# Kernel optimization log

Measured on AMD Instinct MI355X. Metric: run time of the kernel, lower is better.

Reference implementation:

```python
import jax, jax.numpy as jnp
import numpy as np
import math

D_MODEL = 768
N_HEAD = 12
D_FF = 3072
LN_EPS = 1e-5


def gelu_new(x):
    return 0.5 * x * (1.0 + jnp.tanh(jnp.sqrt(2.0 / jnp.pi) * (x + 0.044715 * x ** 3)))


def layer_norm(x, g, b):
    mu = jnp.mean(x, axis=-1, keepdims=True)
    var = jnp.mean(jnp.square(x - mu), axis=-1, keepdims=True)
    return (x - mu) * jax.lax.rsqrt(var + LN_EPS) * g + b


def setup_inputs() -> dict:
    key = jax.random.key(0)
    ks = jax.random.split(key, 8)
    B, S = 4, 2048
    x = jax.random.normal(ks[0], (B, S, D_MODEL), dtype=jnp.float32)
    # causal look-ahead mask: 1 = attend, 0 = masked
    look_ahead_mask = jnp.tril(jnp.ones((S, S), dtype=jnp.float32))[None, None]
    std = 0.02
    Wqkv = jax.random.normal(ks[1], (D_MODEL, 3 * D_MODEL), dtype=jnp.float32) * std
    bqkv = jnp.zeros((3 * D_MODEL,), dtype=jnp.float32)
    Wo = jax.random.normal(ks[2], (D_MODEL, D_MODEL), dtype=jnp.float32) * std
    bo = jnp.zeros((D_MODEL,), dtype=jnp.float32)
    Wfc = jax.random.normal(ks[3], (D_MODEL, D_FF), dtype=jnp.float32) * std
    bfc = jnp.zeros((D_FF,), dtype=jnp.float32)
    Wpr = jax.random.normal(ks[4], (D_FF, D_MODEL), dtype=jnp.float32) * std
    bpr = jnp.zeros((D_MODEL,), dtype=jnp.float32)
    g1 = jnp.ones((D_MODEL,), dtype=jnp.float32)
    b1 = jnp.zeros((D_MODEL,), dtype=jnp.float32)
    g2 = jnp.ones((D_MODEL,), dtype=jnp.float32)
    b2 = jnp.zeros((D_MODEL,), dtype=jnp.float32)
    return dict(x=x, look_ahead_mask=look_ahead_mask, Wqkv=Wqkv, bqkv=bqkv,
                Wo=Wo, bo=bo, Wfc=Wfc, bfc=bfc, Wpr=Wpr, bpr=bpr,
                g1=g1, b1=b1, g2=g2, b2=b2)


def reference(x, look_ahead_mask, Wqkv, bqkv, Wo, bo, Wfc, bfc, Wpr, bpr, g1, b1, g2, b2):
    B, S, D = x.shape
    dk = D // N_HEAD
    # --- attention sublayer (dropout = identity, eval mode) ---
    nx = layer_norm(x, g1, b1)
    qkv = nx @ Wqkv + bqkv                       # [B,S,3D]
    q, k, v = jnp.split(qkv, 3, axis=-1)
    def heads(t):
        return t.reshape(B, S, N_HEAD, dk).transpose(0, 2, 1, 3)  # [B,H,S,dk]
    q, k, v = heads(q), heads(k), heads(v)
    scores = jnp.einsum('bhqd,bhkd->bhqk', q, k) / jnp.sqrt(jnp.float32(dk))
    scores = scores + (1.0 - look_ahead_mask) * -10000.0
    attn_scores = jax.nn.softmax(scores, axis=-1)  # [B,H,S,S]
    out = jnp.einsum('bhqk,bhkd->bhqd', attn_scores, v)
    out = out.transpose(0, 2, 1, 3).reshape(B, S, D)
    a = out @ Wo + bo
    x = x + a
    # --- MLP sublayer ---
    h = layer_norm(x, g2, b2)
    m = gelu_new(h @ Wfc + bfc) @ Wpr + bpr
    x = x + m
    return (x, attn_scores)
```

## Files before the change

kernel.cpp:

```cpp
#include <hip/hip_runtime.h>
#include <stdint.h>

#define D_MODEL 768
#define NHEAD   12
#define DKH     64
#define SEQ     2048
#define BATCH   4
#define DFF     3072
#define NROWS   (BATCH*SEQ)

typedef __bf16 bf16x8 __attribute__((ext_vector_type(8)));
typedef float  f32x4  __attribute__((ext_vector_type(4)));

__device__ __forceinline__ unsigned short f2bf(float f) {
  union { float f; unsigned int u; } v; v.f = f;
  unsigned int r = v.u + 0x7fffu + ((v.u >> 16) & 1u);
  return (unsigned short)(r >> 16);
}

__device__ __forceinline__ void gl_lds16(const void* g, void* l) {
  __builtin_amdgcn_global_load_lds(
      (__attribute__((address_space(1))) void*)(uintptr_t)g,
      (__attribute__((address_space(3))) void*)(uintptr_t)l, 16, 0, 0);
}

__global__ __launch_bounds__(256) void k_prep(
    const float* __restrict__ Wqkv, const float* __restrict__ Wo,
    const float* __restrict__ Wfc, const float* __restrict__ Wpr,
    unsigned short* __restrict__ WqkvT, unsigned short* __restrict__ WoT,
    unsigned short* __restrict__ WfcT, unsigned short* __restrict__ WprT,
    const float* __restrict__ x, const float* __restrict__ g1,
    const float* __restrict__ b1, unsigned short* __restrict__ nx) {
  int id = blockIdx.x;
  if (id < NROWS) {
    int row = id, t = threadIdx.x;
    const float* xr = x + (size_t)row * D_MODEL;
    float v0 = xr[t], v1 = xr[t + 256], v2 = xr[t + 512];
    float s = v0 + v1 + v2;
    float s2 = v0 * v0 + v1 * v1 + v2 * v2;
#pragma unroll
    for (int off = 32; off >= 1; off >>= 1) {
      s  += __shfl_xor(s, off, 64);
      s2 += __shfl_xor(s2, off, 64);
    }
    __shared__ float rs_[4], rs2_[4];
    int w = t >> 6;
    if ((t & 63) == 0) { rs_[w] = s; rs2_[w] = s2; }
    __syncthreads();
    s  = rs_[0] + rs_[1] + rs_[2] + rs_[3];
    s2 = rs2_[0] + rs2_[1] + rs2_[2] + rs2_[3];
    float mu  = s * (1.0f / D_MODEL);
    float var = s2 * (1.0f / D_MODEL) - mu * mu;
    float rstd = rsqrtf(var + 1e-5f);
    unsigned short* yr = nx + (size_t)row * D_MODEL;
    yr[t]       = f2bf((v0 - mu) * rstd * g1[t]       + b1[t]);
    yr[t + 256] = f2bf((v1 - mu) * rstd * g1[t + 256] + b1[t + 256]);
    yr[t + 512] = f2bf((v2 - mu) * rstd * g1[t + 512] + b1[t + 512]);
  } else {
    int wid = id - NROWS;
    const float* W; unsigned short* Wt; int K, N, tid;
    if (wid < 1728)      { W = Wqkv; Wt = WqkvT; K = 768;  N = 2304; tid = wid; }
    else if (wid < 2304) { W = Wo;   Wt = WoT;   K = 768;  N = 768;  tid = wid - 1728; }
    else if (wid < 4608) { W = Wfc;  Wt = WfcT;  K = 768;  N = 3072; tid = wid - 2304; }
    else                 { W = Wpr;  Wt = WprT;  K = 3072; N = 768;  tid = wid - 4608; }
    int ntn = N / 32;
    int n0 = (tid % ntn) * 32, k0 = (tid / ntn) * 32;

    __shared__ float tile[32][33];
    int c = threadIdx.x & 31, r = threadIdx.x >> 5;
#pragma unroll
    for (int i = 0; i < 4; ++i)
      tile[r + i * 8][c] = W[(size_t)(k0 + r + i * 8) * N + n0 + c];
    __syncthreads();
#pragma unroll
    for (int i = 0; i < 4; ++i)
      Wt[(size_t)(n0 + r + i * 8) * K + k0 + c] = f2bf(tile[c][r + i * 8]);
  }
}

__global__ __launch_bounds__(256) void k_ln(const float* __restrict__ x,
                                            const float* __restrict__ g,
                                            const float* __restrict__ bb,
                                            unsigned short* __restrict__ y) {
  int row = blockIdx.x, t = threadIdx.x;
  const float* xr = x + (size_t)row * D_MODEL;
  float v0 = xr[t], v1 = xr[t + 256], v2 = xr[t + 512];
  float s = v0 + v1 + v2;
  float s2 = v0 * v0 + v1 * v1 + v2 * v2;
#pragma unroll
  for (int off = 32; off >= 1; off >>= 1) {
    s  += __shfl_xor(s, off, 64);
    s2 += __shfl_xor(s2, off, 64);
  }
  __shared__ float rs_[4], rs2_[4];
  int w = t >> 6;
  if ((t & 63) == 0) { rs_[w] = s; rs2_[w] = s2; }
  __syncthreads();
  s  = rs_[0] + rs_[1] + rs_[2] + rs_[3];
  s2 = rs2_[0] + rs2_[1] + rs2_[2] + rs2_[3];
  float mu  = s * (1.0f / D_MODEL);
  float var = s2 * (1.0f / D_MODEL) - mu * mu;
  float rstd = rsqrtf(var + 1e-5f);
  unsigned short* yr = y + (size_t)row * D_MODEL;
  yr[t]       = f2bf((v0 - mu) * rstd * g[t]       + bb[t]);
  yr[t + 256] = f2bf((v1 - mu) * rstd * g[t + 256] + bb[t + 256]);
  yr[t + 512] = f2bf((v2 - mu) * rstd * g[t + 512] + bb[t + 512]);
}

#define EPI_QKV 0
#define EPI_WO  1
#define EPI_FC  2
#define EPI_PR  3

template <int EPI>
__global__ __launch_bounds__(256) void k_gemm(
    const unsigned short* __restrict__ A,
    const unsigned short* __restrict__ Bt,
    const float* __restrict__ bias,
    const float* __restrict__ res,
    float* __restrict__ outf,
    unsigned short* __restrict__ outb,
    unsigned short* __restrict__ qo,
    unsigned short* __restrict__ ko,
    unsigned short* __restrict__ vto,
    int K, int N) {
  __shared__ __align__(16) unsigned char smem[36864];
  unsigned short* As = (unsigned short*)smem;
  unsigned short* Bs = (unsigned short*)(smem + 16384);
  int t = threadIdx.x;
  int l = t & 63, w = t >> 6;
  int wm = w >> 1, wn = w & 1;
  int m0 = blockIdx.y * 128, n0 = blockIdx.x * 128;
  int lr = l & 15, lg = l >> 4;

  const f32x4 fz = {0.0f, 0.0f, 0.0f, 0.0f};
  f32x4 acc[4][4];
#pragma unroll
  for (int i = 0; i < 4; ++i)
#pragma unroll
    for (int j = 0; j < 4; ++j) acc[i][j] = fz;

  int arow = t >> 3;
  int aslot = t & 7;
  const unsigned short* Ag = A + (size_t)(m0 + arow) * K + aslot * 8;
  const unsigned short* Bg = Bt + (size_t)(n0 + arow) * K + aslot * 8;
  int ntile = K >> 6;

  for (int kt = 0; kt < ntile; ++kt) {
    const unsigned short* Agk = Ag + kt * 64;
    const unsigned short* Bgk = Bg + kt * 64;
#pragma unroll
    for (int i = 0; i < 4; ++i)
      gl_lds16(Agk + (size_t)i * 32 * K, As + (i * 256 + t) * 8);
#pragma unroll
    for (int i = 0; i < 4; ++i)
      gl_lds16(Bgk + (size_t)i * 32 * K, Bs + (i * 256 + t) * 8);
    __syncthreads();
#pragma unroll
    for (int ks = 0; ks < 2; ++ks) {
      bf16x8 af[4], bf_[4];
#pragma unroll
      for (int i = 0; i < 4; ++i)
        af[i] = *(const bf16x8*)(As + (wm * 64 + i * 16 + lr) * 64 + ks * 32 + lg * 8);
#pragma unroll
      for (int i = 0; i < 4; ++i)
        bf_[i] = *(const bf16x8*)(Bs + (wn * 64 + i * 16 + lr) * 64 + ks * 32 + lg * 8);
#pragma unroll
      for (int i = 0; i < 4; ++i)
#pragma unroll
        for (int j = 0; j < 4; ++j)
          acc[i][j] = __builtin_amdgcn_mfma_f32_16x16x32_bf16(af[i], bf_[j], acc[i][j], 0, 0, 0);
    }
    __syncthreads();
  }

  int mb = m0 + wm * 64;
  int nb = n0 + wn * 64;

  if constexpr (EPI == EPI_WO || EPI == EPI_PR) {
#pragma unroll
    for (int i = 0; i < 4; ++i)
#pragma unroll
      for (int r = 0; r < 4; ++r) {
        int m = mb + i * 16 + 4 * lg + r;
#pragma unroll
        for (int j = 0; j < 4; ++j) {
          int n = nb + j * 16 + lr;
          outf[(size_t)m * D_MODEL + n] = acc[i][j][r] + bias[n] + res[(size_t)m * D_MODEL + n];
        }
      }
  } else if constexpr (EPI == EPI_FC) {
#pragma unroll
    for (int i = 0; i < 4; ++i)
#pragma unroll
      for (int r = 0; r < 4; ++r) {
        int m = mb + i * 16 + 4 * lg + r;
#pragma unroll
        for (int j = 0; j < 4; ++j) {
          int n = nb + j * 16 + lr;
          float u = acc[i][j][r] + bias[n];
          float c = 0.7978845608028654f * (u + 0.044715f * u * u * u);
          float a2 = fabsf(c);
          float e = __expf(-2.0f * a2);
          float th = (1.0f - e) / (1.0f + e);
          th = (c < 0.0f) ? -th : th;
          outb[(size_t)m * DFF + n] = f2bf(0.5f * u * (1.0f + th));
        }
      }
  } else {
    int region = n0 / 768;
    int b = m0 >> 11;
    if (region < 2) {
      unsigned short* dst = (region == 0) ? qo : ko;
#pragma unroll
      for (int i = 0; i < 4; ++i)
#pragma unroll
        for (int r = 0; r < 4; ++r) {
          int m = mb + i * 16 + 4 * lg + r;
          int s = m & (SEQ - 1);
#pragma unroll
          for (int j = 0; j < 4; ++j) {
            int n = nb + j * 16 + lr;
            int nl = n - region * 768;
            int h = nl >> 6, d = nl & 63;
            dst[(((size_t)(b * NHEAD + h) * SEQ + s) << 6) + d] = f2bf(acc[i][j][r] + bias[n]);
          }
        }
    } else {
      int nl = nb - 1536;
      int h = nl >> 6;
      unsigned short* Tw = (unsigned short*)(smem + w * 9216);
#pragma unroll
      for (int j = 0; j < 4; ++j) {
        int dcol = j * 16 + lr;
        int n = nb + j * 16 + lr;
#pragma unroll
        for (int i = 0; i < 4; ++i)
#pragma unroll
          for (int r = 0; r < 4; ++r)
            Tw[dcol * 72 + i * 16 + 4 * lg + r] = f2bf(acc[i][j][r] + bias[n]);
      }
      __syncthreads();
      int srow = l >> 3, sc = (l & 7) * 8;
      int s0 = mb & (SEQ - 1);
#pragma unroll
      for (int i = 0; i < 8; ++i) {
        int d = i * 8 + srow;
        bf16x8 vv = *(const bf16x8*)(Tw + d * 72 + sc);
        *(bf16x8*)(vto + ((size_t)(b * NHEAD + h) * DKH + d) * SEQ + s0 + sc) = vv;
      }
    }
  }
}

template <int WRITEP>
__global__ __launch_bounds__(256) void k_attn(const unsigned short* __restrict__ q,
                                              const unsigned short* __restrict__ kk,
                                              const unsigned short* __restrict__ vt,
                                              float* __restrict__ lsumbuf,
                                              float* __restrict__ attn,
                                              unsigned short* __restrict__ ao) {
  __shared__ __align__(16) unsigned short Ks[2][64 * 64];
  __shared__ __align__(16) unsigned short Vts[2][64 * 64];
  __shared__ __align__(16) unsigned short Pw[4][32 * 72];
  int t = threadIdx.x, l = t & 63, w = t >> 6;
  int lr = l & 15, lg = l >> 4;
  int qt = gridDim.x - 1 - blockIdx.x;
  int bh = blockIdx.y;
  int q0 = qt * 128;
  int qrow0 = q0 + w * 32;
  int kmax = 2 * qt + 1;

  auto stageK = [&](int kt, int buf) {
#pragma unroll
    for (int i = 0; i < 2; ++i) {
      int lin = i * 256 + t;
      gl_lds16(kk + ((size_t)bh * SEQ + kt * 64 + (lin >> 3)) * DKH + (lin & 7) * 8,
               Ks[buf] + lin * 8);
    }
  };
  auto stageV = [&](int kt, int buf) {
#pragma unroll
    for (int i = 0; i < 2; ++i) {
      int lin = i * 256 + t;
      gl_lds16(vt + ((size_t)bh * DKH + (lin >> 3)) * SEQ + kt * 64 + (lin & 7) * 8,
               Vts[buf] + lin * 8);
    }
  };

  bf16x8 aq[2][2];
#pragma unroll
  for (int m = 0; m < 2; ++m) {
    const unsigned short* qbase = q + ((size_t)bh * SEQ + qrow0 + m * 16 + lr) * DKH;
    aq[m][0] = *(const bf16x8*)(qbase + lg * 8);
    aq[m][1] = *(const bf16x8*)(qbase + 32 + lg * 8);
  }

  const f32x4 fz = {0.0f, 0.0f, 0.0f, 0.0f};
  float lsum[2][4] = {{0.f, 0.f, 0.f, 0.f}, {0.f, 0.f, 0.f, 0.f}};
  f32x4 oacc[2][4];
#pragma unroll
  for (int m = 0; m < 2; ++m)
#pragma unroll
    for (int f = 0; f < 4; ++f) oacc[m][f] = fz;

  unsigned short* Pme = Pw[w];
  stageK(0, 0);
  stageV(0, 0);
  __syncthreads();
  int cur = 0;
  for (int kt = 0; kt <= kmax; ++kt) {
    if (kt < kmax) { stageK(kt + 1, cur ^ 1); stageV(kt + 1, cur ^ 1); }
    const unsigned short* Kc = Ks[cur];
    const unsigned short* Vc = Vts[cur];
#pragma unroll
    for (int m = 0; m < 2; ++m) {
      f32x4 sacc[4];
#pragma unroll
      for (int f = 0; f < 4; ++f) sacc[f] = fz;
#pragma unroll
      for (int f = 0; f < 4; ++f) {
        bf16x8 bk0 = *(const bf16x8*)(Kc + (f * 16 + lr) * 64 + lg * 8);
        sacc[f] = __builtin_amdgcn_mfma_f32_16x16x32_bf16(aq[m][0], bk0, sacc[f], 0, 0, 0);
        bf16x8 bk1 = *(const bf16x8*)(Kc + (f * 16 + lr) * 64 + 32 + lg * 8);
        sacc[f] = __builtin_amdgcn_mfma_f32_16x16x32_bf16(aq[m][1], bk1, sacc[f], 0, 0, 0);
      }
#pragma unroll
      for (int r = 0; r < 4; ++r) {
        int qg = qrow0 + m * 16 + 4 * lg + r;
        float rsum = 0.f;
#pragma unroll
        for (int f = 0; f < 4; ++f) {
          int ksg = kt * 64 + f * 16 + lr;
          float p = (ksg <= qg) ? __expf(sacc[f][r] * 0.125f) : 0.0f;
          rsum += p;
          Pme[(m * 16 + 4 * lg + r) * 72 + f * 16 + lr] = f2bf(p);
        }
        rsum += __shfl_xor(rsum, 1, 64);
        rsum += __shfl_xor(rsum, 2, 64);
        rsum += __shfl_xor(rsum, 4, 64);
        rsum += __shfl_xor(rsum, 8, 64);
        lsum[m][r] += rsum;
      }
    }
#pragma unroll
    for (int ds = 0; ds < 2; ++ds)
#pragma unroll
      for (int m = 0; m < 2; ++m) {
        bf16x8 ap = *(const bf16x8*)(Pme + (m * 16 + lr) * 72 + ds * 32 + lg * 8);
#pragma unroll
        for (int f = 0; f < 4; ++f) {
          bf16x8 bv = *(const bf16x8*)(Vc + (f * 16 + lr) * 64 + ds * 32 + lg * 8);
          oacc[m][f] = __builtin_amdgcn_mfma_f32_16x16x32_bf16(ap, bv, oacc[m][f], 0, 0, 0);
        }
      }
    __syncthreads();
    cur ^= 1;
  }

  float invl[2][4];
#pragma unroll
  for (int m = 0; m < 2; ++m)
#pragma unroll
    for (int r = 0; r < 4; ++r) {
      invl[m][r] = 1.0f / lsum[m][r];
      if (WRITEP == 0 && lr == 0)
        lsumbuf[(size_t)bh * SEQ + qrow0 + m * 16 + 4 * lg + r] = lsum[m][r];
    }

  int b = bh / NHEAD, h = bh % NHEAD;
#pragma unroll
  for (int m = 0; m < 2; ++m)
#pragma unroll
    for (int r = 0; r < 4; ++r) {
      int qg = qrow0 + m * 16 + 4 * lg + r;
#pragma unroll
      for (int f = 0; f < 4; ++f)
        ao[(size_t)(b * SEQ + qg) * D_MODEL + h * DKH + f * 16 + lr] =
            f2bf(oacc[m][f][r] * invl[m][r]);
    }

  if (WRITEP) {
    stageK(0, 0);
    __syncthreads();
    cur = 0;
    for (int kt = 0; kt <= kmax; ++kt) {
      if (kt < kmax) stageK(kt + 1, cur ^ 1);
      const unsigned short* Kc = Ks[cur];
#pragma unroll
      for (int m = 0; m < 2; ++m) {
        f32x4 sacc[4];
#pragma unroll
        for (int f = 0; f < 4; ++f) sacc[f] = fz;
#pragma unroll
        for (int f = 0; f < 4; ++f) {
          bf16x8 bk0 = *(const bf16x8*)(Kc + (f * 16 + lr) * 64 + lg * 8);
          sacc[f] = __builtin_amdgcn_mfma_f32_16x16x32_bf16(aq[m][0], bk0, sacc[f], 0, 0, 0);
          bf16x8 bk1 = *(const bf16x8*)(Kc + (f * 16 + lr) * 64 + 32 + lg * 8);
          sacc[f] = __builtin_amdgcn_mfma_f32_16x16x32_bf16(aq[m][1], bk1, sacc[f], 0, 0, 0);
        }
#pragma unroll
        for (int r = 0; r < 4; ++r) {
          int qg = qrow0 + m * 16 + 4 * lg + r;
#pragma unroll
          for (int f = 0; f < 4; ++f) {
            int ksg = kt * 64 + f * 16 + lr;
            float p = (ksg <= qg) ? __expf(sacc[f][r] * 0.125f) * invl[m][r] : 0.0f;
            __builtin_nontemporal_store(p, &attn[((size_t)bh * SEQ + qg) * SEQ + ksg]);
          }
        }
      }
      __syncthreads();
      cur ^= 1;
    }

    int zstart = q0 + 128;
    const f32x4 z4 = {0.f, 0.f, 0.f, 0.f};
#pragma unroll
    for (int m = 0; m < 2; ++m)
#pragma unroll
      for (int r = 0; r < 4; ++r) {
        int qg = qrow0 + m * 16 + 4 * lg + r;
        float* rowp = attn + ((size_t)bh * SEQ + qg) * SEQ;
        for (int c = zstart + lr * 4; c < SEQ; c += 64)
          __builtin_nontemporal_store(z4, (f32x4*)(rowp + c));
      }
  }
}

__global__ __launch_bounds__(256) void k_pwrite(const unsigned short* __restrict__ q,
                                                const unsigned short* __restrict__ kk,
                                                const float* __restrict__ lsumbuf,
                                                float* __restrict__ attn) {
  __shared__ __align__(16) unsigned short Ks[64 * 64];
  int t = threadIdx.x, l = t & 63, w = t >> 6;
  int lr = l & 15, lg = l >> 4;
  int qt = blockIdx.x, bh = blockIdx.y;
  int qrow0 = qt * 64 + w * 16;

  const unsigned short* qbase = q + ((size_t)bh * SEQ + qrow0 + lr) * DKH;
  bf16x8 aq0 = *(const bf16x8*)(qbase + lg * 8);
  bf16x8 aq1 = *(const bf16x8*)(qbase + 32 + lg * 8);

  float invl[4];
#pragma unroll
  for (int r = 0; r < 4; ++r)
    invl[r] = 1.0f / lsumbuf[(size_t)bh * SEQ + qrow0 + 4 * lg + r];

  const f32x4 fz = {0.0f, 0.0f, 0.0f, 0.0f};
  for (int kt = 0; kt <= qt; ++kt) {
#pragma unroll
    for (int i = 0; i < 2; ++i) {
      int lin = i * 256 + t;
      gl_lds16(kk + ((size_t)bh * SEQ + kt * 64 + (lin >> 3)) * DKH + (lin & 7) * 8,
               Ks + lin * 8);
    }
    __syncthreads();
    f32x4 sacc[4];
#pragma unroll
    for (int f = 0; f < 4; ++f) sacc[f] = fz;
#pragma unroll
    for (int f = 0; f < 4; ++f) {
      bf16x8 bk0 = *(const bf16x8*)(Ks + (f * 16 + lr) * 64 + lg * 8);
      sacc[f] = __builtin_amdgcn_mfma_f32_16x16x32_bf16(aq0, bk0, sacc[f], 0, 0, 0);
      bf16x8 bk1 = *(const bf16x8*)(Ks + (f * 16 + lr) * 64 + 32 + lg * 8);
      sacc[f] = __builtin_amdgcn_mfma_f32_16x16x32_bf16(aq1, bk1, sacc[f], 0, 0, 0);
    }
#pragma unroll
    for (int r = 0; r < 4; ++r) {
      int qg = qrow0 + 4 * lg + r;
#pragma unroll
      for (int f = 0; f < 4; ++f) {
        int ksg = kt * 64 + f * 16 + lr;
        float p = (ksg <= qg) ? __expf(sacc[f][r] * 0.125f) * invl[r] : 0.0f;
        attn[((size_t)bh * SEQ + qg) * SEQ + ksg] = p;
      }
    }
    __syncthreads();
  }

  int zstart = (qt + 1) * 64;
#pragma unroll
  for (int r = 0; r < 4; ++r) {
    int qg = qrow0 + 4 * lg + r;
    float* rowp = attn + ((size_t)bh * SEQ + qg) * SEQ;
    for (int c = zstart + lr * 4; c < SEQ; c += 64)
      *(f32x4*)(rowp + c) = fz;
  }
}

extern "C" void kernel_launch(void* const* d_in, const int* in_sizes, int n_in,
                              void* d_out, int out_size, void* d_ws, size_t ws_size,
                              hipStream_t stream) {
  (void)in_sizes; (void)n_in; (void)out_size;
  const float* x    = (const float*)d_in[0];
  const float* Wqkv = (const float*)d_in[2];
  const float* bqkv = (const float*)d_in[3];
  const float* Wo   = (const float*)d_in[4];
  const float* bo   = (const float*)d_in[5];
  const float* Wfc  = (const float*)d_in[6];
  const float* bfc  = (const float*)d_in[7];
  const float* Wpr  = (const float*)d_in[8];
  const float* bpr  = (const float*)d_in[9];
  const float* g1   = (const float*)d_in[10];
  const float* b1   = (const float*)d_in[11];
  const float* g2   = (const float*)d_in[12];
  const float* b2   = (const float*)d_in[13];

  float* outx = (float*)d_out;
  float* attn = outx + (size_t)NROWS * D_MODEL;

  char* ws = (char*)d_ws;
  dim3 blk(256);

  const size_t NEED_FUSED = 77070336;
  if (ws_size >= NEED_FUSED + 65536) {
    unsigned short* qb    = (unsigned short*)(ws + 0);
    unsigned short* kb    = (unsigned short*)(ws + 12582912);
    unsigned short* vtb   = (unsigned short*)(ws + 25165824);
    unsigned short* m1    = (unsigned short*)(ws + 0);
    unsigned short* nx    = (unsigned short*)(ws + 50331648);
    unsigned short* ao    = (unsigned short*)(ws + 50331648);
    unsigned short* hb    = (unsigned short*)(ws + 50331648);
    unsigned short* WqkvT = (unsigned short*)(ws + 62914560);
    unsigned short* WoT   = (unsigned short*)(ws + 66453504);
    unsigned short* WfcT  = (unsigned short*)(ws + 67633152);
    unsigned short* WprT  = (unsigned short*)(ws + 72351744);
    float*          x1    = outx;

    k_prep<<<dim3(NROWS + 6912), blk, 0, stream>>>(
        Wqkv, Wo, Wfc, Wpr, WqkvT, WoT, WfcT, WprT, x, g1, b1, nx);
    k_gemm<EPI_QKV><<<dim3(18, 64), blk, 0, stream>>>(
        nx, WqkvT, bqkv, nullptr, nullptr, nullptr, qb, kb, vtb, 768, 2304);
    k_attn<1><<<dim3(SEQ / 128, BATCH * NHEAD), blk, 0, stream>>>(
        qb, kb, vtb, nullptr, attn, ao);
    k_gemm<EPI_WO><<<dim3(6, 64), blk, 0, stream>>>(
        ao, WoT, bo, x, x1, nullptr, nullptr, nullptr, nullptr, 768, 768);
    k_ln<<<NROWS, blk, 0, stream>>>(x1, g2, b2, hb);
    k_gemm<EPI_FC><<<dim3(24, 64), blk, 0, stream>>>(
        hb, WfcT, bfc, nullptr, nullptr, m1, nullptr, nullptr, nullptr, 768, 3072);
    k_gemm<EPI_PR><<<dim3(6, 64), blk, 0, stream>>>(
        m1, WprT, bpr, x1, outx, nullptr, nullptr, nullptr, nullptr, 3072, 768);
  } else {
    size_t off = 0;
    auto alloc = [&](size_t bytes) {
      char* p = ws + off;
      off += (bytes + 255) & ~(size_t)255;
      return p;
    };
    unsigned short* qb   = (unsigned short*)alloc((size_t)NROWS * D_MODEL * 2);
    unsigned short* kb   = (unsigned short*)alloc((size_t)NROWS * D_MODEL * 2);
    float*          lsum = (float*)alloc((size_t)BATCH * NHEAD * SEQ * 4);

    char* aws = (char*)attn;
    size_t aoff = 0;
    auto aalloc = [&](size_t bytes) {
      char* p = aws + aoff;
      aoff += (bytes + 255) & ~(size_t)255;
      return p;
    };
    unsigned short* WqkvT = (unsigned short*)aalloc((size_t)2304 * 768 * 2);
    unsigned short* WoT   = (unsigned short*)aalloc((size_t)768 * 768 * 2);
    unsigned short* WfcT  = (unsigned short*)aalloc((size_t)3072 * 768 * 2);
    unsigned short* WprT  = (unsigned short*)aalloc((size_t)768 * 3072 * 2);
    unsigned short* nx    = (unsigned short*)aalloc((size_t)NROWS * D_MODEL * 2);
    unsigned short* vtb   = (unsigned short*)aalloc((size_t)NROWS * D_MODEL * 2);
    unsigned short* ao    = (unsigned short*)aalloc((size_t)NROWS * D_MODEL * 2);
    float*          x1    = (float*)aalloc((size_t)NROWS * D_MODEL * 4);
    unsigned short* hb    = (unsigned short*)aalloc((size_t)NROWS * D_MODEL * 2);
    unsigned short* m1    = (unsigned short*)aalloc((size_t)NROWS * DFF * 2);

    k_prep<<<dim3(NROWS + 6912), blk, 0, stream>>>(
        Wqkv, Wo, Wfc, Wpr, WqkvT, WoT, WfcT, WprT, x, g1, b1, nx);
    k_gemm<EPI_QKV><<<dim3(18, 64), blk, 0, stream>>>(
        nx, WqkvT, bqkv, nullptr, nullptr, nullptr, qb, kb, vtb, 768, 2304);
    k_attn<0><<<dim3(SEQ / 128, BATCH * NHEAD), blk, 0, stream>>>(
        qb, kb, vtb, lsum, nullptr, ao);
    k_gemm<EPI_WO><<<dim3(6, 64), blk, 0, stream>>>(
        ao, WoT, bo, x, x1, nullptr, nullptr, nullptr, nullptr, 768, 768);
    k_ln<<<NROWS, blk, 0, stream>>>(x1, g2, b2, hb);
    k_gemm<EPI_FC><<<dim3(24, 64), blk, 0, stream>>>(
        hb, WfcT, bfc, nullptr, nullptr, m1, nullptr, nullptr, nullptr, 768, 3072);
    k_gemm<EPI_PR><<<dim3(6, 64), blk, 0, stream>>>(
        m1, WprT, bpr, x1, outx, nullptr, nullptr, nullptr, nullptr, 3072, 768);

    k_pwrite<<<dim3(SEQ / 64, BATCH * NHEAD), blk, 0, stream>>>(qb, kb, lsum, attn);
  }
}
```

Baseline: 529.9 us.

## Transpose score MFMA for vectorized attention-prob stores and swizzle GEMM block order

Measured after the change: 611.5 us. +15.4%, slower.

```diff
diff --git a/kernel.cpp b/kernel.cpp
--- a/kernel.cpp
+++ b/kernel.cpp
@@ -130,7 +130,13 @@
   int t = threadIdx.x;
   int l = t & 63, w = t >> 6;
   int wm = w >> 1, wn = w & 1;
-  int m0 = blockIdx.y * 128, n0 = blockIdx.x * 128;
+
+  int gx = gridDim.x;
+  int nwg = gx * gridDim.y;
+  int orig = blockIdx.y * gx + blockIdx.x;
+  int wg = (orig & 7) * (nwg >> 3) + (orig >> 3);
+  int bx = wg % gx, by = wg / gx;
+  int m0 = by * 128, n0 = bx * 128;
   int lr = l & 15, lg = l >> 4;
 
   const f32x4 fz = {0.0f, 0.0f, 0.0f, 0.0f};
@@ -263,6 +269,7 @@
   __shared__ __align__(16) unsigned short Ks[2][64 * 64];
   __shared__ __align__(16) unsigned short Vts[2][64 * 64];
   __shared__ __align__(16) unsigned short Pw[4][32 * 72];
+  __shared__ float invs[4][32];
   int t = threadIdx.x, l = t & 63, w = t >> 6;
   int lr = l & 15, lg = l >> 4;
   int qt = gridDim.x - 1 - blockIdx.x;
@@ -367,6 +374,13 @@
       if (WRITEP == 0 && lr == 0)
         lsumbuf[(size_t)bh * SEQ + qrow0 + m * 16 + 4 * lg + r] = lsum[m][r];
     }
+  if (WRITEP && lr == 0) {
+#pragma unroll
+    for (int m = 0; m < 2; ++m)
+#pragma unroll
+      for (int r = 0; r < 4; ++r)
+        invs[w][m * 16 + 4 * lg + r] = invl[m][r];
+  }
 
   int b = bh / NHEAD, h = bh % NHEAD;
 #pragma unroll
@@ -381,12 +395,22 @@
     }
 
   if (WRITEP) {
+    float invp[2];
+#pragma unroll
+    for (int m = 0; m < 2; ++m) invp[m] = invs[w][m * 16 + lr];
+
     stageK(0, 0);
     __syncthreads();
     cur = 0;
     for (int kt = 0; kt <= kmax; ++kt) {
       if (kt < kmax) stageK(kt + 1, cur ^ 1);
       const unsigned short* Kc = Ks[cur];
+      bf16x8 bkf[4][2];
+#pragma unroll
+      for (int f = 0; f < 4; ++f) {
+        bkf[f][0] = *(const bf16x8*)(Kc + (f * 16 + lr) * 64 + lg * 8);
+        bkf[f][1] = *(const bf16x8*)(Kc + (f * 16 + lr) * 64 + 32 + lg * 8);
+      }
 #pragma unroll
       for (int m = 0; m < 2; ++m) {
         f32x4 sacc[4];
@@ -394,20 +418,19 @@
         for (int f = 0; f < 4; ++f) sacc[f] = fz;
 #pragma unroll
         for (int f = 0; f < 4; ++f) {
-          bf16x8 bk0 = *(const bf16x8*)(Kc + (f * 16 + lr) * 64 + lg * 8);
-          sacc[f] = __builtin_amdgcn_mfma_f32_16x16x32_bf16(aq[m][0], bk0, sacc[f], 0, 0, 0);
-          bf16x8 bk1 = *(const bf16x8*)(Kc + (f * 16 + lr) * 64 + 32 + lg * 8);
-          sacc[f] = __builtin_amdgcn_mfma_f32_16x16x32_bf16(aq[m][1], bk1, sacc[f], 0, 0, 0);
+          sacc[f] = __builtin_amdgcn_mfma_f32_16x16x32_bf16(bkf[f][0], aq[m][0], sacc[f], 0, 0, 0);
+          sacc[f] = __builtin_amdgcn_mfma_f32_16x16x32_bf16(bkf[f][1], aq[m][1], sacc[f], 0, 0, 0);
         }
-#pragma unroll
-        for (int r = 0; r < 4; ++r) {
-          int qg = qrow0 + m * 16 + 4 * lg + r;
-#pragma unroll
-          for (int f = 0; f < 4; ++f) {
-            int ksg = kt * 64 + f * 16 + lr;
-            float p = (ksg <= qg) ? __expf(sacc[f][r] * 0.125f) * invl[m][r] : 0.0f;
-            __builtin_nontemporal_store(p, &attn[((size_t)bh * SEQ + qg) * SEQ + ksg]);
-          }
+        int qg = qrow0 + m * 16 + lr;
+        float* rowp = attn + ((size_t)bh * SEQ + qg) * SEQ;
+#pragma unroll
+        for (int f = 0; f < 4; ++f) {
+          int kbase = kt * 64 + f * 16 + 4 * lg;
+          f32x4 pq;
+#pragma unroll
+          for (int r = 0; r < 4; ++r)
+            pq[r] = (kbase + r <= qg) ? __expf(sacc[f][r] * 0.125f) * invp[m] : 0.0f;
+          __builtin_nontemporal_store(pq, (f32x4*)(rowp + kbase));
         }
       }
       __syncthreads();
@@ -417,14 +440,12 @@
     int zstart = q0 + 128;
     const f32x4 z4 = {0.f, 0.f, 0.f, 0.f};
 #pragma unroll
-    for (int m = 0; m < 2; ++m)
-#pragma unroll
-      for (int r = 0; r < 4; ++r) {
-        int qg = qrow0 + m * 16 + 4 * lg + r;
-        float* rowp = attn + ((size_t)bh * SEQ + qg) * SEQ;
-        for (int c = zstart + lr * 4; c < SEQ; c += 64)
-          __builtin_nontemporal_store(z4, (f32x4*)(rowp + c));
-      }
+    for (int m = 0; m < 2; ++m) {
+      int qg = qrow0 + m * 16 + lr;
+      float* rowp = attn + ((size_t)bh * SEQ + qg) * SEQ;
+      for (int c = zstart + lg * 4; c < SEQ; c += 16)
+        __builtin_nontemporal_store(z4, (f32x4*)(rowp + c));
+    }
   }
 }
 
```
